# Performance work log

Measured on AMD Instinct MI355X. Metric: run time of the kernel, lower is better.

The kernel has to match this reference:

```python
import jax, jax.numpy as jnp
import numpy as np

B = 8
C_IN = 3
DIV = 7
N0 = 20 * 4 ** DIV      # 327680 pixels at division 7
N1 = N0 // 4            # 81920 pixels at division 6
N2 = N1 // 4            # 20480 pixels at division 5
K_CONV = 10             # SpherePHD conv kernel size (triangle + 9 neighbors)
K_ADJ = 4               # pooling neighborhood (pixel + 3 edge-adjacent)


def setup_inputs() -> dict:
    key = jax.random.key(0)
    ks = jax.random.split(key, 15)
    x = jax.random.normal(ks[0], (B, C_IN, N0), dtype=jnp.float32)
    conv_t0 = jax.random.randint(ks[1], (N0, K_CONV), 0, N0, dtype=jnp.int32)
    conv_t1 = jax.random.randint(ks[2], (N1, K_CONV), 0, N1, dtype=jnp.int32)
    conv_t2 = jax.random.randint(ks[3], (N2, K_CONV), 0, N2, dtype=jnp.int32)
    adj0 = jax.random.randint(ks[4], (N0, K_ADJ), 0, N0, dtype=jnp.int32)
    adj1 = jax.random.randint(ks[5], (N1, K_ADJ), 0, N1, dtype=jnp.int32)
    pool0 = jax.random.randint(ks[6], (N1,), 0, N0, dtype=jnp.int32)
    pool1 = jax.random.randint(ks[7], (N2,), 0, N1, dtype=jnp.int32)
    w1 = jax.random.normal(ks[8], (16, C_IN, K_CONV), dtype=jnp.float32) * 0.1
    b1 = jax.random.normal(ks[9], (16,), dtype=jnp.float32) * 0.1
    w2 = jax.random.normal(ks[10], (32, 16, K_CONV), dtype=jnp.float32) * 0.1
    b2 = jax.random.normal(ks[11], (32,), dtype=jnp.float32) * 0.1
    w3 = jax.random.normal(ks[12], (10, 32, K_CONV), dtype=jnp.float32) * 0.1
    b3 = jax.random.normal(ks[13], (10,), dtype=jnp.float32) * 0.1
    return {"x": x, "conv_t0": conv_t0, "conv_t1": conv_t1, "conv_t2": conv_t2,
            "adj0": adj0, "adj1": adj1, "pool0": pool0, "pool1": pool1,
            "w1": w1, "b1": b1, "w2": w2, "b2": b2, "w3": w3, "b3": b3}


def phd_conv2d(x, table, w, b):
    # x: [B, Cin, N]; table: [N, K] neighbor indices; w: [Cout, Cin, K]
    g = x[:, :, table]                               # gather -> [B, Cin, N, K]
    return jnp.einsum('bcnk,ock->bon', g, w) + b[None, :, None]


def phd_maxpool(x, adj, pool):
    # max over adjacency neighborhood, then 4:1 downsample via pooling table
    m = jnp.max(x[:, :, adj], axis=-1)               # [B, C, N_fine]
    return m[:, :, pool]                             # [B, C, N_coarse]


def reference(x, conv_t0, conv_t1, conv_t2, adj0, adj1, pool0, pool1,
              w1, b1, w2, b2, w3, b3):
    h = phd_conv2d(x, conv_t0, w1, b1)               # [B, 16, N0]
    h = phd_maxpool(h, adj0, pool0)                  # [B, 16, N1]
    h = phd_conv2d(h, conv_t1, w2, b2)               # [B, 32, N1]
    h = phd_maxpool(h, adj1, pool1)                  # [B, 32, N2]
    h = phd_conv2d(h, conv_t2, w3, b3)               # [B, 10, N2]
    return jnp.mean(h, axis=-1)                      # PHD_avgpool -> [B, 10]
```

## Files before the change

### kernel.cpp

```cpp
#include <hip/hip_runtime.h>

#define NB 8
#define CIN 3
#define N0 327680
#define N1 81920
#define N2 20480
#define KC 10
#define KA 4

typedef __attribute__((ext_vector_type(8))) short bf16x8;
typedef __attribute__((ext_vector_type(4))) float f32x4;
typedef uint4 __attribute__((aligned(4))) uint4_u;
typedef int4  __attribute__((aligned(4))) int4_u;

__device__ __forceinline__ unsigned f2bf(float f) {
  unsigned u = __float_as_uint(f);
  return (u + 0x7FFFu + ((u >> 16) & 1u)) >> 16;
}

union bfrag { bf16x8 v; unsigned u[4]; };

__global__ __launch_bounds__(256) void kpre(
    const float* __restrict__ x, uint4* __restrict__ xT12,
    const int* __restrict__ conv_t0, const int* __restrict__ conv_t1,
    const int* __restrict__ conv_t2,
    const int* __restrict__ adj0, const int* __restrict__ adj1,
    const int* __restrict__ pool0, const int* __restrict__ pool1,
    int* __restrict__ fidxM, int* __restrict__ fidxP, float* __restrict__ A12,
    const float* __restrict__ w1, const float* __restrict__ w2,
    const float* __restrict__ w3, const float* __restrict__ b3,
    unsigned short* __restrict__ wB1, unsigned short* __restrict__ wB,
    float* __restrict__ w3t, float* __restrict__ out) {
  int blk = blockIdx.x;
  if (blk < 1280) {
    int bp = blk & 3;
    int t = (blk >> 2) * 256 + threadIdx.x;
    int n = t * 4;
    const float* p0 = x + (size_t)(2 * bp) * CIN * N0 + n;
    const float* p1 = p0 + (size_t)CIN * N0;
    float4 a0 = *(const float4*)(p0);
    float4 a1 = *(const float4*)(p0 + N0);
    float4 a2 = *(const float4*)(p0 + 2 * N0);
    float4 c0 = *(const float4*)(p1);
    float4 c1 = *(const float4*)(p1 + N0);
    float4 c2 = *(const float4*)(p1 + 2 * N0);
    unsigned w[12];
    const float* A0 = &a0.x; const float* A1 = &a1.x; const float* A2 = &a2.x;
    const float* C0 = &c0.x; const float* C1 = &c1.x; const float* C2 = &c2.x;
#pragma unroll
    for (int r = 0; r < 4; ++r) {
      w[r * 3 + 0] = f2bf(A0[r]) | (f2bf(A1[r]) << 16);
      w[r * 3 + 1] = f2bf(A2[r]) | (f2bf(C0[r]) << 16);
      w[r * 3 + 2] = f2bf(C1[r]) | (f2bf(C2[r]) << 16);
    }
    uint4* dst = xT12 + ((size_t)bp * N0 / 4 + t) * 3;
    dst[0] = make_uint4(w[0], w[1], w[2], w[3]);
    dst[1] = make_uint4(w[4], w[5], w[6], w[7]);
    dst[2] = make_uint4(w[8], w[9], w[10], w[11]);
  } else if (blk < 2560) {
    int t = (blk - 1280) * 256 + threadIdx.x;
    int j = t >> 2, p = t & 3;
    int pj = pool0[j];
    int pos = adj0[pj * KA + p];
    const int2* s0 = (const int2*)(conv_t0 + (size_t)pos * 10);
    int2 q0 = s0[0], q1 = s0[1], q2 = s0[2], q3 = s0[3], q4 = s0[4];
    int4_u* dM = (int4_u*)(fidxM + (size_t)t * 12);
    dM[0] = make_int4(q0.x * 12, q0.y * 12, q4.x * 12, q4.y * 12);
    dM[1] = make_int4(q1.x * 12, q1.y * 12, q2.x * 12, q2.y * 12);
    dM[2] = make_int4(q3.x * 12, q3.y * 12, 0, 0);
    if (j < N2) {
      int qj = pool1[j];
      int qos = adj1[qj * KA + p];
      const int2* s1 = (const int2*)(conv_t1 + (size_t)qos * 10);
      int2 r0 = s1[0], r1 = s1[1], r2 = s1[2], r3 = s1[3], r4 = s1[4];
      int4_u* dP = (int4_u*)(fidxP + (size_t)t * 12);
      dP[0] = make_int4(r0.x * 32, r1.x * 32, r2.x * 32, r3.x * 32);
      dP[1] = make_int4(r4.x * 32, 0,          r0.y * 32, r1.y * 32);
      dP[2] = make_int4(r2.y * 32, r3.y * 32, r4.y * 32, 0);
    }
  } else if (blk < 3360) {
    int t = (blk - 2560) * 256 + threadIdx.x;
    int n = conv_t2[t];
    int k = t % 10;
    atomicAdd(&A12[n * 12 + k], 1.0f);
  } else {
    int t = (blk - 3360) * 256 + threadIdx.x;
    if (t < 1024) {
      int ch = t >> 9, rest = t & 511, l = rest >> 3, e = rest & 7;
      int k = ch * 32 + ((l >> 4) * 8) + e;
      int tap = k >> 2, cc = k & 3;
      float v = (tap < KC && cc < CIN) ? w1[((l & 15) * CIN + cc) * KC + tap] : 0.f;
      wB1[t] = (unsigned short)f2bf(v);
    }
    if (t < 5120) {
      int e = t & 7, l = (t >> 3) & 63, nt = (t >> 9) & 1, q = t >> 10;
      int kc = q * 32 + ((l >> 4) * 8) + e;
      int tap = kc >> 4, c = kc & 15;
      int o = nt * 16 + (l & 15);
      wB[t] = (unsigned short)f2bf(w2[(o * 16 + c) * KC + tap]);
    }
    if (t < 3200) { int o = t % 10, r = t / 10, c = r & 31, k = r >> 5;
                    w3t[t] = w3[(o * 32 + c) * KC + k]; }
    if (t < 80)   out[t] = b3[t % 10];
  }
}

__global__ __launch_bounds__(256, 4) void k1(
    const char* __restrict__ xT12, const int* __restrict__ fidxM,
    const bf16x8* __restrict__ wB1, const float* __restrict__ b1,
    unsigned short* __restrict__ h2) {
  int blk = blockIdx.x;
  int bp = blk & 3;
  int wave = threadIdx.x >> 6;
  int lane = threadIdx.x & 63;
  int col = lane & 15, hi = lane >> 4;
  int tile0 = ((blk >> 2) * 4 + wave) * 4;
  const char* xb = xT12 + (size_t)bp * N0 * 12;
  unsigned short* h2b0 = h2 + (size_t)(2 * bp) * N1 * 16;
  unsigned short* h2b1 = h2b0 + (size_t)N1 * 16;
  bf16x8 B0 = wB1[lane];
  bf16x8 B1 = wB1[64 + lane];
  float bias = b1[col];
  int seloff = ((hi + 1) >> 1) << 2;

  int4 I[4];
#pragma unroll
  for (int i = 0; i < 4; ++i)
    I[i] = *(const int4_u*)(fidxM + ((size_t)(tile0 + i) * 16 + col) * 12 + seloff);

  uint4 g[4][4];
#pragma unroll
  for (int i = 0; i < 4; ++i) {
    int a0 = (hi == 2) ? I[i].z : I[i].x;
    int a1 = (hi == 2) ? I[i].w : I[i].y;
    int a2 = (hi == 0) ? I[i].z : 0;
    int a3 = (hi == 0) ? I[i].w : 0;
    g[i][0] = *(const uint4_u*)(xb + a0);
    g[i][1] = *(const uint4_u*)(xb + a1);
    g[i][2] = *(const uint4_u*)(xb + a2);
    g[i][3] = *(const uint4_u*)(xb + a3);
  }
  __builtin_amdgcn_sched_barrier(0);

#pragma unroll
  for (int i = 0; i < 4; ++i) {
    uint4 g0 = g[i][0], g1 = g[i][1], g2 = g[i][2], g3 = g[i][3];
    bfrag A0c0, A1c0, A0c1, A1c1;
    A0c0.u[0] = g0.x; A0c0.u[1] = g0.y & 0xFFFFu;
    A0c0.u[2] = g1.x; A0c0.u[3] = g1.y & 0xFFFFu;
    A1c0.u[0] = (g0.y >> 16) | (g0.z << 16); A1c0.u[1] = g0.z >> 16;
    A1c0.u[2] = (g1.y >> 16) | (g1.z << 16); A1c0.u[3] = g1.z >> 16;
    A0c1.u[0] = g2.x; A0c1.u[1] = g2.y & 0xFFFFu;
    A0c1.u[2] = g3.x; A0c1.u[3] = g3.y & 0xFFFFu;
    A1c1.u[0] = (g2.y >> 16) | (g2.z << 16); A1c1.u[1] = g2.z >> 16;
    A1c1.u[2] = (g3.y >> 16) | (g3.z << 16); A1c1.u[3] = g3.z >> 16;
    f32x4 z = {0.f, 0.f, 0.f, 0.f};
    f32x4 acc0 = __builtin_amdgcn_mfma_f32_16x16x32_bf16(A0c0.v, B0, z, 0, 0, 0);
    acc0 = __builtin_amdgcn_mfma_f32_16x16x32_bf16(A0c1.v, B1, acc0, 0, 0, 0);
    f32x4 acc1 = __builtin_amdgcn_mfma_f32_16x16x32_bf16(A1c0.v, B0, z, 0, 0, 0);
    acc1 = __builtin_amdgcn_mfma_f32_16x16x32_bf16(A1c1.v, B1, acc1, 0, 0, 0);
    float m0 = fmaxf(fmaxf(acc0[0], acc0[1]), fmaxf(acc0[2], acc0[3])) + bias;
    float m1 = fmaxf(fmaxf(acc1[0], acc1[1]), fmaxf(acc1[2], acc1[3])) + bias;
    size_t j = (size_t)(tile0 + i) * 4 + hi;
    h2b0[j * 16 + col] = (unsigned short)f2bf(m0);
    h2b1[j * 16 + col] = (unsigned short)f2bf(m1);
  }
}

__global__ __launch_bounds__(256) void k2(
    const char* __restrict__ h2, const int* __restrict__ fidxP,
    const bf16x8* __restrict__ wB, const float* __restrict__ b2,
    float* __restrict__ h3) {
  int blk = blockIdx.x;
  int b = blk & 7;
  int wave = threadIdx.x >> 6;
  int lane = threadIdx.x & 63;
  int col = lane & 15;
  int odd = (lane >> 5) & 1;
  int tile0 = ((blk >> 3) * 4 + wave) * 8;
  const char* hb = h2 + (size_t)b * N1 * 32 + ((lane >> 4) & 1) * 16;

  bf16x8 Bf[10];
#pragma unroll
  for (int i = 0; i < 10; ++i) Bf[i] = wB[i * 64 + lane];
  float bias0 = b2[col];
  float bias1 = b2[16 + col];

#pragma unroll 2
  for (int i = 0; i < 8; ++i) {
    int tile = tile0 + i;
    const int* fp = fidxP + ((size_t)tile * 16 + col) * 12 + odd * 6;
    int4 T = *(const int4_u*)fp;
    int  T4 = fp[4];
    f32x4 acc0 = {0.f, 0.f, 0.f, 0.f};
    f32x4 acc1 = {0.f, 0.f, 0.f, 0.f};
    bf16x8 A;
    A = *(const bf16x8*)(hb + T.x);
    acc0 = __builtin_amdgcn_mfma_f32_16x16x32_bf16(A, Bf[0], acc0, 0, 0, 0);
    acc1 = __builtin_amdgcn_mfma_f32_16x16x32_bf16(A, Bf[1], acc1, 0, 0, 0);
    A = *(const bf16x8*)(hb + T.y);
    acc0 = __builtin_amdgcn_mfma_f32_16x16x32_bf16(A, Bf[2], acc0, 0, 0, 0);
    acc1 = __builtin_amdgcn_mfma_f32_16x16x32_bf16(A, Bf[3], acc1, 0, 0, 0);
    A = *(const bf16x8*)(hb + T.z);
    acc0 = __builtin_amdgcn_mfma_f32_16x16x32_bf16(A, Bf[4], acc0, 0, 0, 0);
    acc1 = __builtin_amdgcn_mfma_f32_16x16x32_bf16(A, Bf[5], acc1, 0, 0, 0);
    A = *(const bf16x8*)(hb + T.w);
    acc0 = __builtin_amdgcn_mfma_f32_16x16x32_bf16(A, Bf[6], acc0, 0, 0, 0);
    acc1 = __builtin_amdgcn_mfma_f32_16x16x32_bf16(A, Bf[7], acc1, 0, 0, 0);
    A = *(const bf16x8*)(hb + T4);
    acc0 = __builtin_amdgcn_mfma_f32_16x16x32_bf16(A, Bf[8], acc0, 0, 0, 0);
    acc1 = __builtin_amdgcn_mfma_f32_16x16x32_bf16(A, Bf[9], acc1, 0, 0, 0);
    float m0 = fmaxf(fmaxf(acc0[0], acc0[1]), fmaxf(acc0[2], acc0[3])) + bias0;
    float m1 = fmaxf(fmaxf(acc1[0], acc1[1]), fmaxf(acc1[2], acc1[3])) + bias1;
    int j = tile * 4 + (lane >> 4);
    float* dst = h3 + ((size_t)b * N2 + j) * 32 + col;
    dst[0]  = m0;
    dst[16] = m1;
  }
}

#define K3B_NCH 256
__global__ __launch_bounds__(256) void k3b(
    const float* __restrict__ h3, const float* __restrict__ A12,
    float* __restrict__ G) {
  __shared__ float SA[K3B_NCH * 12];
  __shared__ float GL[320];
  int blk = blockIdx.x;
  int b = blk & 7;
  int n0 = (blk >> 3) * K3B_NCH;
  int tid = threadIdx.x;
  const float4* src = (const float4*)(A12 + (size_t)n0 * 12);
#pragma unroll
  for (int i = 0; i < 3; ++i)
    ((float4*)SA)[tid + i * 256] = src[tid + i * 256];
  for (int i = tid; i < 320; i += 256) GL[i] = 0.f;
  __syncthreads();
  int wave = tid >> 6, lane = tid & 63;
  int c = lane & 31, nh = lane >> 5;
  float acc[10];
#pragma unroll
  for (int o = 0; o < 10; ++o) acc[o] = 0.f;
#pragma unroll 4
  for (int s = 0; s < K3B_NCH / 8; ++s) {
    int nl = s * 8 + wave * 2 + nh;
    float hv = h3[((size_t)b * N2 + n0 + nl) * 32 + c];
    const float4* ar = (const float4*)(SA + nl * 12);
    float4 a0 = ar[0], a1 = ar[1], a2 = ar[2];
    acc[0] += hv * a0.x; acc[1] += hv * a0.y;
    acc[2] += hv * a0.z; acc[3] += hv * a0.w;
    acc[4] += hv * a1.x; acc[5] += hv * a1.y;
    acc[6] += hv * a1.z; acc[7] += hv * a1.w;
    acc[8] += hv * a2.x; acc[9] += hv * a2.y;
  }
#pragma unroll
  for (int o = 0; o < 10; ++o) acc[o] += __shfl_xor(acc[o], 32);
  if (lane < 32) {
#pragma unroll
    for (int o = 0; o < 10; ++o) atomicAdd(&GL[c * 10 + o], acc[o]);
  }
  __syncthreads();
  for (int i = tid; i < 320; i += 256)
    atomicAdd(&G[b * 320 + i], GL[i]);
}

__global__ __launch_bounds__(256) void k3c(
    const float* __restrict__ G, const float* __restrict__ w3t,
    float* __restrict__ out) {
  int t = blockIdx.x * 256 + threadIdx.x;
  int pair = t >> 5, c = t & 31;
  int b = pair / 10, o = pair % 10;
  float s = 0.f;
#pragma unroll
  for (int k = 0; k < KC; ++k)
    s += G[b * 320 + c * 10 + k] * w3t[k * 320 + c * 10 + o];
#pragma unroll
  for (int off = 1; off < 32; off <<= 1) s += __shfl_xor(s, off);
  if ((threadIdx.x & 31) == 0) atomicAdd(&out[pair], s * (1.0f / N2));
}

extern "C" void kernel_launch(void* const* d_in, const int* in_sizes, int n_in,
                              void* d_out, int out_size, void* d_ws, size_t ws_size,
                              hipStream_t stream) {
  const float* x       = (const float*)d_in[0];
  const int*   conv_t0 = (const int*)d_in[1];
  const int*   conv_t1 = (const int*)d_in[2];
  const int*   conv_t2 = (const int*)d_in[3];
  const int*   adj0    = (const int*)d_in[4];
  const int*   adj1    = (const int*)d_in[5];
  const int*   pool0   = (const int*)d_in[6];
  const int*   pool1   = (const int*)d_in[7];
  const float* w1      = (const float*)d_in[8];
  const float* b1      = (const float*)d_in[9];
  const float* w2      = (const float*)d_in[10];
  const float* b2      = (const float*)d_in[11];
  const float* w3      = (const float*)d_in[12];
  const float* b3      = (const float*)d_in[13];
  float* out  = (float*)d_out;
  float* wsf  = (float*)d_ws;

  float* h3b   = wsf;
  uint4* xT12  = (uint4*)wsf;
  unsigned short* h2b = (unsigned short*)(wsf + 5242880);
  int* fidxM   = (int*)(wsf + 2 * 5242880);
  int* fidxP   = fidxM + (size_t)N1 * 4 * 12;
  float* A12   = (float*)(fidxP + (size_t)N2 * 4 * 12);
  float* G     = A12 + (size_t)N2 * 12;
  unsigned short* wB1 = (unsigned short*)(G + 2560);
  unsigned short* wB  = wB1 + 1024;
  float* w3t   = (float*)(wB + 5120);

  hipMemsetAsync(A12, 0, (size_t)(N2 * 12 + 2560) * 4, stream);
  kpre<<<3380, 256, 0, stream>>>(x, xT12, conv_t0, conv_t1, conv_t2,
                                 adj0, adj1, pool0, pool1,
                                 fidxM, fidxP, A12,
                                 w1, w2, w3, b3, wB1, wB, w3t, out);
  k1<<<5120, 256, 0, stream>>>((const char*)xT12, fidxM, (const bf16x8*)wB1, b1, h2b);
  k2<<<1280, 256, 0, stream>>>((const char*)h2b, fidxP, (const bf16x8*)wB, b2, h3b);
  k3b<<<8 * (N2 / K3B_NCH), 256, 0, stream>>>(h3b, A12, G);
  k3c<<<10, 256, 0, stream>>>(G, w3t, out);
}
```

Baseline: 156.9 us.

## Pack all batches per pixel into 64-byte rows and share gathers across batch pairs

The transposed input is reorganized so each pixel stores all 8 batches' 3 channels as bf16 in one 64-byte aligned row, instead of one 12-byte record per batch pair. Conv1 kernel k1 now gathers each neighbor row once and runs the MFMA/maxpool for all four batch pairs from registers. This reuses the index loads and row fetches across batches, and with 4x fewer blocks it cuts the number of separate scattered accesses. In exchange, the packed buffer is padded to 64 bytes per pixel, so more bytes are written and more registers are live per thread, and the occupancy hint from launch bounds is dropped.

Measured after the change: 154.6 us. No clear change (-1.5%).

```diff
diff --git a/kernel.cpp b/kernel.cpp
--- a/kernel.cpp
+++ b/kernel.cpp
@@ -10,7 +10,6 @@
 
 typedef __attribute__((ext_vector_type(8))) short bf16x8;
 typedef __attribute__((ext_vector_type(4))) float f32x4;
-typedef uint4 __attribute__((aligned(4))) uint4_u;
 typedef int4  __attribute__((aligned(4))) int4_u;
 
 __device__ __forceinline__ unsigned f2bf(float f) {
@@ -21,7 +20,7 @@
 union bfrag { bf16x8 v; unsigned u[4]; };
 
 __global__ __launch_bounds__(256) void kpre(
-    const float* __restrict__ x, uint4* __restrict__ xT12,
+    const float* __restrict__ x, uint4* __restrict__ xT64,
     const int* __restrict__ conv_t0, const int* __restrict__ conv_t1,
     const int* __restrict__ conv_t2,
     const int* __restrict__ adj0, const int* __restrict__ adj1,
@@ -33,30 +32,23 @@
     float* __restrict__ w3t, float* __restrict__ out) {
   int blk = blockIdx.x;
   if (blk < 1280) {
-    int bp = blk & 3;
-    int t = (blk >> 2) * 256 + threadIdx.x;
-    int n = t * 4;
-    const float* p0 = x + (size_t)(2 * bp) * CIN * N0 + n;
-    const float* p1 = p0 + (size_t)CIN * N0;
-    float4 a0 = *(const float4*)(p0);
-    float4 a1 = *(const float4*)(p0 + N0);
-    float4 a2 = *(const float4*)(p0 + 2 * N0);
-    float4 c0 = *(const float4*)(p1);
-    float4 c1 = *(const float4*)(p1 + N0);
-    float4 c2 = *(const float4*)(p1 + 2 * N0);
-    unsigned w[12];
-    const float* A0 = &a0.x; const float* A1 = &a1.x; const float* A2 = &a2.x;
-    const float* C0 = &c0.x; const float* C1 = &c1.x; const float* C2 = &c2.x;
-#pragma unroll
-    for (int r = 0; r < 4; ++r) {
-      w[r * 3 + 0] = f2bf(A0[r]) | (f2bf(A1[r]) << 16);
-      w[r * 3 + 1] = f2bf(A2[r]) | (f2bf(C0[r]) << 16);
-      w[r * 3 + 2] = f2bf(C1[r]) | (f2bf(C2[r]) << 16);
-    }
-    uint4* dst = xT12 + ((size_t)bp * N0 / 4 + t) * 3;
-    dst[0] = make_uint4(w[0], w[1], w[2], w[3]);
-    dst[1] = make_uint4(w[4], w[5], w[6], w[7]);
-    dst[2] = make_uint4(w[8], w[9], w[10], w[11]);
+    int n = blk * 256 + threadIdx.x;
+    unsigned d[12];
+#pragma unroll
+    for (int bp = 0; bp < 4; ++bp) {
+      const float* pe = x + (size_t)(2 * bp) * CIN * N0 + n;
+      const float* po = pe + (size_t)CIN * N0;
+      float e0 = pe[0], e1 = pe[N0], e2 = pe[2 * N0];
+      float o0 = po[0], o1 = po[N0], o2 = po[2 * N0];
+      d[bp * 3 + 0] = f2bf(e0) | (f2bf(e1) << 16);
+      d[bp * 3 + 1] = f2bf(e2) | (f2bf(o0) << 16);
+      d[bp * 3 + 2] = f2bf(o1) | (f2bf(o2) << 16);
+    }
+    uint4* dst = xT64 + (size_t)n * 4;
+    dst[0] = make_uint4(d[0], d[1], d[2], d[3]);
+    dst[1] = make_uint4(d[4], d[5], d[6], d[7]);
+    dst[2] = make_uint4(d[8], d[9], d[10], d[11]);
+    dst[3] = make_uint4(0, 0, 0, 0);
   } else if (blk < 2560) {
     int t = (blk - 1280) * 256 + threadIdx.x;
     int j = t >> 2, p = t & 3;
@@ -65,9 +57,9 @@
     const int2* s0 = (const int2*)(conv_t0 + (size_t)pos * 10);
     int2 q0 = s0[0], q1 = s0[1], q2 = s0[2], q3 = s0[3], q4 = s0[4];
     int4_u* dM = (int4_u*)(fidxM + (size_t)t * 12);
-    dM[0] = make_int4(q0.x * 12, q0.y * 12, q4.x * 12, q4.y * 12);
-    dM[1] = make_int4(q1.x * 12, q1.y * 12, q2.x * 12, q2.y * 12);
-    dM[2] = make_int4(q3.x * 12, q3.y * 12, 0, 0);
+    dM[0] = make_int4(q0.x * 64, q0.y * 64, q4.x * 64, q4.y * 64);
+    dM[1] = make_int4(q1.x * 64, q1.y * 64, q2.x * 64, q2.y * 64);
+    dM[2] = make_int4(q3.x * 64, q3.y * 64, 0, 0);
     if (j < N2) {
       int qj = pool1[j];
       int qos = adj1[qj * KA + p];
@@ -105,65 +97,78 @@
   }
 }
 
-__global__ __launch_bounds__(256, 4) void k1(
-    const char* __restrict__ xT12, const int* __restrict__ fidxM,
+#define TR0(s) ((s) == 0 ? Ra.x : (s) == 1 ? Ra.w : (s) == 2 ? Rb.z : Rc.y)
+#define TR1(s) ((s) == 0 ? Ra.y : (s) == 1 ? Rb.x : (s) == 2 ? Rb.w : Rc.z)
+#define TR2(s) ((s) == 0 ? Ra.z : (s) == 1 ? Rb.y : (s) == 2 ? Rc.x : Rc.w)
+
+__global__ __launch_bounds__(256) void k1(
+    const char* __restrict__ xT64, const int* __restrict__ fidxM,
     const bf16x8* __restrict__ wB1, const float* __restrict__ b1,
     unsigned short* __restrict__ h2) {
   int blk = blockIdx.x;
-  int bp = blk & 3;
   int wave = threadIdx.x >> 6;
   int lane = threadIdx.x & 63;
   int col = lane & 15, hi = lane >> 4;
-  int tile0 = ((blk >> 2) * 4 + wave) * 4;
-  const char* xb = xT12 + (size_t)bp * N0 * 12;
-  unsigned short* h2b0 = h2 + (size_t)(2 * bp) * N1 * 16;
-  unsigned short* h2b1 = h2b0 + (size_t)N1 * 16;
+  int tile0 = (blk * 4 + wave) * 4;
   bf16x8 B0 = wB1[lane];
   bf16x8 B1 = wB1[64 + lane];
   float bias = b1[col];
   int seloff = ((hi + 1) >> 1) << 2;
 
-  int4 I[4];
-#pragma unroll
-  for (int i = 0; i < 4; ++i)
-    I[i] = *(const int4_u*)(fidxM + ((size_t)(tile0 + i) * 16 + col) * 12 + seloff);
-
-  uint4 g[4][4];
 #pragma unroll
   for (int i = 0; i < 4; ++i) {
-    int a0 = (hi == 2) ? I[i].z : I[i].x;
-    int a1 = (hi == 2) ? I[i].w : I[i].y;
-    int a2 = (hi == 0) ? I[i].z : 0;
-    int a3 = (hi == 0) ? I[i].w : 0;
-    g[i][0] = *(const uint4_u*)(xb + a0);
-    g[i][1] = *(const uint4_u*)(xb + a1);
-    g[i][2] = *(const uint4_u*)(xb + a2);
-    g[i][3] = *(const uint4_u*)(xb + a3);
-  }
-  __builtin_amdgcn_sched_barrier(0);
-
-#pragma unroll
-  for (int i = 0; i < 4; ++i) {
-    uint4 g0 = g[i][0], g1 = g[i][1], g2 = g[i][2], g3 = g[i][3];
-    bfrag A0c0, A1c0, A0c1, A1c1;
-    A0c0.u[0] = g0.x; A0c0.u[1] = g0.y & 0xFFFFu;
-    A0c0.u[2] = g1.x; A0c0.u[3] = g1.y & 0xFFFFu;
-    A1c0.u[0] = (g0.y >> 16) | (g0.z << 16); A1c0.u[1] = g0.z >> 16;
-    A1c0.u[2] = (g1.y >> 16) | (g1.z << 16); A1c0.u[3] = g1.z >> 16;
-    A0c1.u[0] = g2.x; A0c1.u[1] = g2.y & 0xFFFFu;
-    A0c1.u[2] = g3.x; A0c1.u[3] = g3.y & 0xFFFFu;
-    A1c1.u[0] = (g2.y >> 16) | (g2.z << 16); A1c1.u[1] = g2.z >> 16;
-    A1c1.u[2] = (g3.y >> 16) | (g3.z << 16); A1c1.u[3] = g3.z >> 16;
-    f32x4 z = {0.f, 0.f, 0.f, 0.f};
-    f32x4 acc0 = __builtin_amdgcn_mfma_f32_16x16x32_bf16(A0c0.v, B0, z, 0, 0, 0);
-    acc0 = __builtin_amdgcn_mfma_f32_16x16x32_bf16(A0c1.v, B1, acc0, 0, 0, 0);
-    f32x4 acc1 = __builtin_amdgcn_mfma_f32_16x16x32_bf16(A1c0.v, B0, z, 0, 0, 0);
-    acc1 = __builtin_amdgcn_mfma_f32_16x16x32_bf16(A1c1.v, B1, acc1, 0, 0, 0);
-    float m0 = fmaxf(fmaxf(acc0[0], acc0[1]), fmaxf(acc0[2], acc0[3])) + bias;
-    float m1 = fmaxf(fmaxf(acc1[0], acc1[1]), fmaxf(acc1[2], acc1[3])) + bias;
-    size_t j = (size_t)(tile0 + i) * 4 + hi;
-    h2b0[j * 16 + col] = (unsigned short)f2bf(m0);
-    h2b1[j * 16 + col] = (unsigned short)f2bf(m1);
+    int tile = tile0 + i;
+    int4 I = *(const int4_u*)(fidxM + ((size_t)tile * 16 + col) * 12 + seloff);
+    int a0 = (hi == 2) ? I.z : I.x;
+    int a1 = (hi == 2) ? I.w : I.y;
+    int a2 = (hi == 0) ? I.z : 0;
+    int a3 = (hi == 0) ? I.w : 0;
+    const uint4* r0p = (const uint4*)(xT64 + a0);
+    const uint4* r1p = (const uint4*)(xT64 + a1);
+    const uint4* r2p = (const uint4*)(xT64 + a2);
+    const uint4* r3p = (const uint4*)(xT64 + a3);
+    uint4 R0a = r0p[0], R0b = r0p[1], R0c = r0p[2];
+    uint4 R1a = r1p[0], R1b = r1p[1], R1c = r1p[2];
+    uint4 R2a = r2p[0], R2b = r2p[1], R2c = r2p[2];
+    uint4 R3a = r3p[0], R3b = r3p[1], R3c = r3p[2];
+    size_t j = (size_t)tile * 4 + hi;
+    unsigned short* dst = h2 + j * 16 + col;
+
+#define DO_BPAIR(s)                                                           \
+    {                                                                         \
+      unsigned t0, t1, t2, u0, u1, u2, v0, v1, v2, w0, w1, w2;                \
+      { uint4 Ra = R0a, Rb = R0b, Rc = R0c;                                   \
+        t0 = TR0(s); t1 = TR1(s); t2 = TR2(s); }                              \
+      { uint4 Ra = R1a, Rb = R1b, Rc = R1c;                                   \
+        u0 = TR0(s); u1 = TR1(s); u2 = TR2(s); }                              \
+      { uint4 Ra = R2a, Rb = R2b, Rc = R2c;                                   \
+        v0 = TR0(s); v1 = TR1(s); v2 = TR2(s); }                              \
+      { uint4 Ra = R3a, Rb = R3b, Rc = R3c;                                   \
+        w0 = TR0(s); w1 = TR1(s); w2 = TR2(s); }                              \
+      bfrag A0c0, A1c0, A0c1, A1c1;                                           \
+      A0c0.u[0] = t0; A0c0.u[1] = t1 & 0xFFFFu;                               \
+      A0c0.u[2] = u0; A0c0.u[3] = u1 & 0xFFFFu;                               \
+      A1c0.u[0] = (t1 >> 16) | (t2 << 16); A1c0.u[1] = t2 >> 16;              \
+      A1c0.u[2] = (u1 >> 16) | (u2 << 16); A1c0.u[3] = u2 >> 16;              \
+      A0c1.u[0] = v0; A0c1.u[1] = v1 & 0xFFFFu;                               \
+      A0c1.u[2] = w0; A0c1.u[3] = w1 & 0xFFFFu;                               \
+      A1c1.u[0] = (v1 >> 16) | (v2 << 16); A1c1.u[1] = v2 >> 16;              \
+      A1c1.u[2] = (w1 >> 16) | (w2 << 16); A1c1.u[3] = w2 >> 16;              \
+      f32x4 z = {0.f, 0.f, 0.f, 0.f};                                         \
+      f32x4 acc0 = __builtin_amdgcn_mfma_f32_16x16x32_bf16(A0c0.v, B0, z, 0, 0, 0); \
+      acc0 = __builtin_amdgcn_mfma_f32_16x16x32_bf16(A0c1.v, B1, acc0, 0, 0, 0);    \
+      f32x4 acc1 = __builtin_amdgcn_mfma_f32_16x16x32_bf16(A1c0.v, B0, z, 0, 0, 0); \
+      acc1 = __builtin_amdgcn_mfma_f32_16x16x32_bf16(A1c1.v, B1, acc1, 0, 0, 0);    \
+      float m0 = fmaxf(fmaxf(acc0[0], acc0[1]), fmaxf(acc0[2], acc0[3])) + bias;    \
+      float m1 = fmaxf(fmaxf(acc1[0], acc1[1]), fmaxf(acc1[2], acc1[3])) + bias;    \
+      dst[(size_t)(2 * (s)) * N1 * 16]     = (unsigned short)f2bf(m0);        \
+      dst[(size_t)(2 * (s) + 1) * N1 * 16] = (unsigned short)f2bf(m1);        \
+    }
+    DO_BPAIR(0)
+    DO_BPAIR(1)
+    DO_BPAIR(2)
+    DO_BPAIR(3)
+#undef DO_BPAIR
   }
 }
 
@@ -299,7 +304,7 @@
   float* wsf  = (float*)d_ws;
 
   float* h3b   = wsf;
-  uint4* xT12  = (uint4*)wsf;
+  uint4* xT64  = (uint4*)wsf;
   unsigned short* h2b = (unsigned short*)(wsf + 5242880);
   int* fidxM   = (int*)(wsf + 2 * 5242880);
   int* fidxP   = fidxM + (size_t)N1 * 4 * 12;
@@ -310,11 +315,11 @@
   float* w3t   = (float*)(wB + 5120);
 
   hipMemsetAsync(A12, 0, (size_t)(N2 * 12 + 2560) * 4, stream);
-  kpre<<<3380, 256, 0, stream>>>(x, xT12, conv_t0, conv_t1, conv_t2,
+  kpre<<<3380, 256, 0, stream>>>(x, xT64, conv_t0, conv_t1, conv_t2,
                                  adj0, adj1, pool0, pool1,
                                  fidxM, fidxP, A12,
                                  w1, w2, w3, b3, wB1, wB, w3t, out);
-  k1<<<5120, 256, 0, stream>>>((const char*)xT12, fidxM, (const bf16x8*)wB1, b1, h2b);
+  k1<<<1280, 256, 0, stream>>>((const char*)xT64, fidxM, (const bf16x8*)wB1, b1, h2b);
   k2<<<1280, 256, 0, stream>>>((const char*)h2b, fidxP, (const bf16x8*)wB, b2, h3b);
   k3b<<<8 * (N2 / K3B_NCH), 256, 0, stream>>>(h3b, A12, G);
   k3c<<<10, 256, 0, stream>>>(G, w3t, out);
```
